# Kernel optimization log

Measured on AMD Instinct MI355X. Metric: run time of the kernel, lower is better.

Reference implementation:

```python
import jax, jax.numpy as jnp
import numpy as np

B, S, D, H = 8, 1024, 768, 12
DH = D // H
EPS = 1e-5


def setup_inputs() -> dict:
    key = jax.random.key(0)
    ks = jax.random.split(key, 12)
    sc_h = 1.0 / np.sqrt(DH)
    sc_d = 1.0 / np.sqrt(D)
    return {
        "x": jax.random.normal(ks[0], (B, S, D), jnp.float32),
        "ln1_g": jnp.ones((D,), jnp.float32),
        "ln1_b": jnp.zeros((D,), jnp.float32),
        "Wq": jax.random.normal(ks[1], (H, DH, DH), jnp.float32) * sc_h,
        "bq": jax.random.normal(ks[2], (H, DH), jnp.float32) * 0.01,
        "Wk": jax.random.normal(ks[3], (H, DH, DH), jnp.float32) * sc_h,
        "bk": jax.random.normal(ks[4], (H, DH), jnp.float32) * 0.01,
        "Wv": jax.random.normal(ks[5], (H, DH, DH), jnp.float32) * sc_h,
        "bv": jax.random.normal(ks[6], (H, DH), jnp.float32) * 0.01,
        "ln2_g": jnp.ones((D,), jnp.float32),
        "ln2_b": jnp.zeros((D,), jnp.float32),
        "W1": jax.random.normal(ks[7], (D, 4 * D), jnp.float32) * sc_d,  # c_fc (bias=False)
        "W2": jax.random.normal(ks[8], (4 * D, D), jnp.float32) * (1.0 / np.sqrt(4 * D)),  # c_proj (bias=False)
    }


def _layernorm(x, g, b):
    m = jnp.mean(x, axis=-1, keepdims=True)
    v = jnp.mean(jnp.square(x - m), axis=-1, keepdims=True)
    return (x - m) * jax.lax.rsqrt(v + EPS) * g + b


def _msa(x, Wq, bq, Wk, bk, Wv, bv):
    b, s, d = x.shape
    h = x.reshape(b, s, H, DH)  # per-head slices of the embedding
    q = jnp.einsum('bshd,hde->bhse', h, Wq) + bq[None, :, None, :]
    k = jnp.einsum('bshd,hde->bhse', h, Wk) + bk[None, :, None, :]
    v = jnp.einsum('bshd,hde->bhse', h, Wv) + bv[None, :, None, :]
    scores = jnp.einsum('bhse,bhte->bhst', q, k) / np.sqrt(DH).astype(np.float32)
    attn = jax.nn.softmax(scores, axis=-1)
    o = jnp.einsum('bhst,bhte->bhse', attn, v)
    return o.transpose(0, 2, 1, 3).reshape(b, s, d)  # concat heads


def reference(x, ln1_g, ln1_b, Wq, bq, Wk, bk, Wv, bv, ln2_g, ln2_b, W1, W2):
    out = x + _msa(_layernorm(x, ln1_g, ln1_b), Wq, bq, Wk, bk, Wv, bv)
    h = _layernorm(out, ln2_g, ln2_b)
    ffn = jnp.dot(jax.nn.gelu(jnp.dot(h, W1), approximate=False), W2)
    return out + ffn
```

## Files before the change

kernel.cpp:

```cpp
#include <hip/hip_runtime.h>
#include <hip/hip_bf16.h>
#include <math.h>

#define B_ 8
#define S_ 1024
#define D_ 768
#define H_ 12
#define QSCALE 0.18033688011112042f

typedef __attribute__((ext_vector_type(8))) short short8;
typedef __attribute__((ext_vector_type(4))) float floatx4;
typedef unsigned short ushort_t;

__device__ __forceinline__ ushort_t f2bf(float f) {
  unsigned int u = __builtin_bit_cast(unsigned int, f);
  u += 0x7fffu + ((u >> 16) & 1u);
  return (ushort_t)(u >> 16);
}

__device__ __forceinline__ unsigned int pkbf(float a, float b) {
  __hip_bfloat162 h = __float22bfloat162_rn(make_float2(a, b));
  unsigned int r;
  __builtin_memcpy(&r, &h, sizeof(r));
  return r;
}

__global__ __launch_bounds__(256) void ln_bf16(
    const float* __restrict__ in, const float* __restrict__ g,
    const float* __restrict__ bias, ushort_t* __restrict__ out) {
  const int row = blockIdx.x * 4 + (threadIdx.x >> 6);
  const int lane = threadIdx.x & 63;
  const float* p = in + (size_t)row * D_;
  float4 v[3];
#pragma unroll
  for (int j = 0; j < 3; ++j) v[j] = *(const float4*)(p + j * 256 + lane * 4);
  float s = 0.f;
#pragma unroll
  for (int j = 0; j < 3; ++j) s += (v[j].x + v[j].y) + (v[j].z + v[j].w);
#pragma unroll
  for (int m = 1; m < 64; m <<= 1) s += __shfl_xor(s, m);
  const float mean = s * (1.0f / D_);
  float q = 0.f;
#pragma unroll
  for (int j = 0; j < 3; ++j) {
    const float a = v[j].x - mean, b = v[j].y - mean;
    const float c = v[j].z - mean, d = v[j].w - mean;
    q += (a * a + b * b) + (c * c + d * d);
  }
#pragma unroll
  for (int m = 1; m < 64; m <<= 1) q += __shfl_xor(q, m);
  const float rstd = rsqrtf(q * (1.0f / D_) + 1e-5f);
  ushort_t* o = out + (size_t)row * D_;
#pragma unroll
  for (int j = 0; j < 3; ++j) {
    const float4 gv = *(const float4*)(g + j * 256 + lane * 4);
    const float4 bv = *(const float4*)(bias + j * 256 + lane * 4);
    const unsigned int p01 = pkbf((v[j].x - mean) * rstd * gv.x + bv.x,
                                  (v[j].y - mean) * rstd * gv.y + bv.y);
    const unsigned int p23 = pkbf((v[j].z - mean) * rstd * gv.z + bv.z,
                                  (v[j].w - mean) * rstd * gv.w + bv.w);
    *(uint2*)(o + j * 256 + lane * 4) = make_uint2(p01, p23);
  }
}

__global__ __launch_bounds__(256) void transpose_cast(
    const float* __restrict__ W, ushort_t* __restrict__ Wt, int Kdim, int Ndim) {
  __shared__ float tile[32][33];
  const int n0 = blockIdx.x * 32, k0 = blockIdx.y * 32;
  const int tx = threadIdx.x & 31, ty = threadIdx.x >> 5;
#pragma unroll
  for (int i = 0; i < 32; i += 8)
    tile[ty + i][tx] = W[(size_t)(k0 + ty + i) * Ndim + n0 + tx];
  __syncthreads();
#pragma unroll
  for (int i = 0; i < 32; i += 8)
    Wt[(size_t)(n0 + ty + i) * Kdim + k0 + tx] = f2bf(tile[tx][ty + i]);
}

__global__ __launch_bounds__(256) void trans_w64(
    const float* __restrict__ Wq, const float* __restrict__ Wk,
    const float* __restrict__ Wv, ushort_t* __restrict__ Wqt,
    ushort_t* __restrict__ Wkt, ushort_t* __restrict__ Wvt) {
  const int h = blockIdx.x;
  const float* W = blockIdx.y == 0 ? Wq : blockIdx.y == 1 ? Wk : Wv;
  ushort_t* O = blockIdx.y == 0 ? Wqt : blockIdx.y == 1 ? Wkt : Wvt;
  __shared__ float t[64][65];
  const int tid = threadIdx.x;
#pragma unroll
  for (int i = 0; i < 16; ++i) {
    const int idx = tid + i * 256;
    t[idx >> 6][idx & 63] = W[h * 4096 + idx];
  }
  __syncthreads();
#pragma unroll
  for (int i = 0; i < 16; ++i) {
    const int idx = tid + i * 256;
    O[h * 4096 + idx] = f2bf(t[idx & 63][idx >> 6]);
  }
}

__global__ __launch_bounds__(256) void qkv_mfma(
    const ushort_t* __restrict__ xbf,
    const ushort_t* __restrict__ Wqt, const ushort_t* __restrict__ Wkt,
    const ushort_t* __restrict__ Wvt,
    const float* __restrict__ bq, const float* __restrict__ bk,
    const float* __restrict__ bv,
    ushort_t* __restrict__ qo, ushort_t* __restrict__ ko,
    ushort_t* __restrict__ vt) {
  const int h = blockIdx.y;
  const int mb = blockIdx.x * 128;
  const int tid = threadIdx.x;
  const int wave = tid >> 6, lane = tid & 63;
  const int lc = lane & 15, kq = lane >> 4;
  const int wm = wave * 32;

  short8 af[2][2];
#pragma unroll
  for (int mi = 0; mi < 2; ++mi)
#pragma unroll
    for (int kc = 0; kc < 2; ++kc)
      af[mi][kc] = *(const short8*)(xbf + (size_t)(mb + wm + mi * 16 + lc) * D_ +
                                    h * 64 + kc * 32 + kq * 8);

  const ushort_t* Wp[3] = {Wqt + h * 4096, Wkt + h * 4096, Wvt + h * 4096};
  floatx4 acc[3][2][4] = {};
#pragma unroll
  for (int w3 = 0; w3 < 3; ++w3)
#pragma unroll
    for (int n = 0; n < 4; ++n)
#pragma unroll
      for (int kc = 0; kc < 2; ++kc) {
        const short8 bfv =
            *(const short8*)(Wp[w3] + (n * 16 + lc) * 64 + kc * 32 + kq * 8);
#pragma unroll
        for (int mi = 0; mi < 2; ++mi)
          acc[w3][mi][n] = __builtin_amdgcn_mfma_f32_16x16x32_bf16(
              af[mi][kc], bfv, acc[w3][mi][n], 0, 0, 0);
      }

  const int b = mb >> 10;
  const size_t obase = (size_t)(b * H_ + h) * (S_ * 64);
#pragma unroll
  for (int w3 = 0; w3 < 2; ++w3) {
    const float* bias = (w3 == 0 ? bq : bk) + h * 64;
    ushort_t* outp = w3 == 0 ? qo : ko;
#pragma unroll
    for (int n = 0; n < 4; ++n) {
      const int e = n * 16 + lc;
      const float bvv = bias[e];
#pragma unroll
      for (int mi = 0; mi < 2; ++mi)
#pragma unroll
        for (int r = 0; r < 4; ++r) {
          const int sl = (mb & 1023) + wm + mi * 16 + kq * 4 + r;
          float v = acc[w3][mi][n][r] + bvv;
          if (w3 == 0) v *= QSCALE;
          outp[obase + (size_t)sl * 64 + e] = f2bf(v);
        }
    }
  }
#pragma unroll
  for (int n = 0; n < 4; ++n) {
    const int e = n * 16 + lc;
    const float bvv = bv[h * 64 + e];
#pragma unroll
    for (int mi = 0; mi < 2; ++mi) {
      const int sl0 = (mb & 1023) + wm + mi * 16 + kq * 4;
      const unsigned int p01 =
          pkbf(acc[2][mi][n][0] + bvv, acc[2][mi][n][1] + bvv);
      const unsigned int p23 =
          pkbf(acc[2][mi][n][2] + bvv, acc[2][mi][n][3] + bvv);
      *(uint2*)(vt + obase + (size_t)e * S_ + sl0) = make_uint2(p01, p23);
    }
  }
}

__global__ __launch_bounds__(256) void attn_mfma(
    const ushort_t* __restrict__ qb, const ushort_t* __restrict__ kb,
    const ushort_t* __restrict__ vt, const float* __restrict__ x,
    float* __restrict__ out1) {
  const int bh = blockIdx.x;
  const int tid = threadIdx.x;
  const int wave = tid >> 6, lane = tid & 63;
  const int lc = lane & 15, kq = lane >> 4;
  const int q0 = blockIdx.y * 128 + wave * 32;

  __shared__ __align__(16) ushort_t Ks[64 * 64];
  __shared__ __align__(16) ushort_t Vs[64 * 64];
  __shared__ __align__(16) ushort_t Pw[4][2][16 * 72];

  const ushort_t* qp = qb + (size_t)bh * (S_ * 64);
  const ushort_t* kp = kb + (size_t)bh * (S_ * 64);
  const ushort_t* vp = vt + (size_t)bh * (S_ * 64);

  short8 qf[2][2];
#pragma unroll
  for (int qi = 0; qi < 2; ++qi)
#pragma unroll
    for (int kc = 0; kc < 2; ++kc)
      qf[qi][kc] = *(const short8*)(qp + (size_t)(q0 + qi * 16 + lc) * 64 +
                                    kc * 32 + kq * 8);

  const int srow = tid >> 3;
  const int sgc = ((tid & 7) ^ (srow & 7)) * 8;
  const int slds = srow * 64 + (tid & 7) * 8;
  const int swz = lc & 7;

  float l_r[2] = {0.0f, 0.0f};
  floatx4 oacc[2][4] = {};

  for (int kt = 0; kt < 16; ++kt) {
#pragma unroll
    for (int half = 0; half < 2; ++half) {
      const int r = half * 32 + srow;
      __builtin_amdgcn_global_load_lds(
          (const __attribute__((address_space(1))) unsigned int*)
              (kp + (size_t)(kt * 64 + r) * 64 + sgc),
          (__attribute__((address_space(3))) unsigned int*)
              (Ks + half * 2048 + slds), 16, 0, 0);
      __builtin_amdgcn_global_load_lds(
          (const __attribute__((address_space(1))) unsigned int*)
              (vp + (size_t)r * S_ + kt * 64 + sgc),
          (__attribute__((address_space(3))) unsigned int*)
              (Vs + half * 2048 + slds), 16, 0, 0);
    }
    __syncthreads();

    floatx4 sacc[2][4] = {};
#pragma unroll
    for (int mi = 0; mi < 4; ++mi) {
      const int row = (mi * 16 + lc) * 64;
#pragma unroll
      for (int kc = 0; kc < 2; ++kc) {
        const short8 kf =
            *(const short8*)(Ks + row + ((kc * 4 + kq) ^ swz) * 8);
        sacc[0][mi] = __builtin_amdgcn_mfma_f32_16x16x32_bf16(
            kf, qf[0][kc], sacc[0][mi], 0, 0, 0);
        sacc[1][mi] = __builtin_amdgcn_mfma_f32_16x16x32_bf16(
            kf, qf[1][kc], sacc[1][mi], 0, 0, 0);
      }
    }

#pragma unroll
    for (int qi = 0; qi < 2; ++qi) {
      float pr[4][4];
      float sm = 0.f;
#pragma unroll
      for (int mi = 0; mi < 4; ++mi)
#pragma unroll
        for (int r = 0; r < 4; ++r) {
          pr[mi][r] = exp2f(sacc[qi][mi][r]);
          sm += pr[mi][r];
        }
      l_r[qi] += sm;
#pragma unroll
      for (int mi = 0; mi < 4; ++mi) {
        const unsigned int p01 = pkbf(pr[mi][0], pr[mi][1]);
        const unsigned int p23 = pkbf(pr[mi][2], pr[mi][3]);
        *(uint2*)(&Pw[wave][qi][lc * 72 + mi * 16 + kq * 4]) =
            make_uint2(p01, p23);
      }
    }
    asm volatile("s_waitcnt lgkmcnt(0)" ::: "memory");

    short8 pf[2][2];
#pragma unroll
    for (int qi = 0; qi < 2; ++qi)
#pragma unroll
      for (int kc = 0; kc < 2; ++kc)
        pf[qi][kc] =
            *(const short8*)(&Pw[wave][qi][lc * 72 + kc * 32 + kq * 8]);
#pragma unroll
    for (int mi = 0; mi < 4; ++mi) {
      const int row = (mi * 16 + lc) * 64;
#pragma unroll
      for (int kc = 0; kc < 2; ++kc) {
        const short8 vf =
            *(const short8*)(Vs + row + ((kc * 4 + kq) ^ swz) * 8);
        oacc[0][mi] = __builtin_amdgcn_mfma_f32_16x16x32_bf16(
            vf, pf[0][kc], oacc[0][mi], 0, 0, 0);
        oacc[1][mi] = __builtin_amdgcn_mfma_f32_16x16x32_bf16(
            vf, pf[1][kc], oacc[1][mi], 0, 0, 0);
      }
    }
    __syncthreads();
  }

  const int b = bh / H_, h = bh % H_;
  float* Ow = (float*)&Pw[wave][0][0];
#pragma unroll
  for (int qi = 0; qi < 2; ++qi) {
    float lt = l_r[qi];
    lt += __shfl_xor(lt, 16);
    lt += __shfl_xor(lt, 32);
    const float inv = 1.0f / lt;
#pragma unroll
    for (int mi = 0; mi < 4; ++mi) {
      floatx4 ov = oacc[qi][mi];
      ov[0] *= inv; ov[1] *= inv; ov[2] *= inv; ov[3] *= inv;
      *(floatx4*)(&Ow[lc * 68 + mi * 16 + kq * 4]) = ov;
    }
    asm volatile("s_waitcnt lgkmcnt(0)" ::: "memory");
    const int row = (lane >> 3) & 7, c8 = (lane & 7) * 4;
#pragma unroll
    for (int rg = 0; rg < 2; ++rg) {
      const int qq = rg * 8 + row;
      const size_t gbase =
          ((size_t)(b * S_) + q0 + qi * 16 + qq) * D_ + h * 64 + c8;
#pragma unroll
      for (int j = 0; j < 2; ++j) {
        const float4 ov = *(const float4*)(&Ow[qq * 68 + j * 32 + c8]);
        const float4 xv = *(const float4*)(x + gbase + j * 32);
        *(float4*)(out1 + gbase + j * 32) =
            make_float4(ov.x + xv.x, ov.y + xv.y, ov.z + xv.z, ov.w + xv.w);
      }
    }
    asm volatile("s_waitcnt lgkmcnt(0)" ::: "memory");
  }
}

template <int N, int K, bool GELU, bool RESID, bool OUT_BF16>
__global__ __launch_bounds__(256) void mfma_gemm(
    const ushort_t* __restrict__ A, const ushort_t* __restrict__ Bt,
    const float* __restrict__ resid, void* __restrict__ Cout) {
  const int mb = blockIdx.y * 128;
  const int nb = blockIdx.x * 128;
  const int tid = threadIdx.x;
  const int wave = tid >> 6, lane = tid & 63;
  const int wm = (wave >> 1) * 64, wn = (wave & 1) * 64;

  __shared__ ushort_t Asp[128 * 32];
  __shared__ ushort_t Bsp[128 * 32];

  const int srow = wave * 16 + (lane >> 2);
  const int skoff = (lane & 3) * 8;

  floatx4 acc[4][4] = {};

  for (int kb = 0; kb < K; kb += 32) {
#pragma unroll
    for (int j = 0; j < 2; ++j) {
      const int row = j * 64 + srow;
      __builtin_amdgcn_global_load_lds(
          (const __attribute__((address_space(1))) unsigned int*)
              (A + (size_t)(mb + row) * K + kb + skoff),
          (__attribute__((address_space(3))) unsigned int*)
              (Asp + (size_t)row * 32 + skoff),
          16, 0, 0);
      __builtin_amdgcn_global_load_lds(
          (const __attribute__((address_space(1))) unsigned int*)
              (Bt + (size_t)(nb + row) * K + kb + skoff),
          (__attribute__((address_space(3))) unsigned int*)
              (Bsp + (size_t)row * 32 + skoff),
          16, 0, 0);
    }
    __syncthreads();

    const short8* As8 = (const short8*)Asp;
    const short8* Bs8 = (const short8*)Bsp;
    const int lrow = lane & 15, lkq = lane >> 4;
    short8 af[4], bfr[4];
#pragma unroll
    for (int i = 0; i < 4; ++i) {
      af[i]  = As8[(wm + i * 16 + lrow) * 4 + lkq];
      bfr[i] = Bs8[(wn + i * 16 + lrow) * 4 + lkq];
    }
#pragma unroll
    for (int i = 0; i < 4; ++i)
#pragma unroll
      for (int j = 0; j < 4; ++j)
        acc[i][j] = __builtin_amdgcn_mfma_f32_16x16x32_bf16(
            af[i], bfr[j], acc[i][j], 0, 0, 0);
    __syncthreads();
  }

  const int lcol = lane & 15, lr4 = (lane >> 4) * 4;
#pragma unroll
  for (int i = 0; i < 4; ++i)
#pragma unroll
    for (int r = 0; r < 4; ++r) {
      const int m = mb + wm + i * 16 + lr4 + r;
#pragma unroll
      for (int j = 0; j < 4; ++j) {
        const int col = nb + wn + j * 16 + lcol;
        float vv = acc[i][j][r];
        if (GELU) vv = 0.5f * vv * (1.0f + erff(vv * 0.70710678f));
        if (RESID) vv += resid[(size_t)m * N + col];
        if (OUT_BF16)
          ((ushort_t*)Cout)[(size_t)m * N + col] = f2bf(vv);
        else
          ((float*)Cout)[(size_t)m * N + col] = vv;
      }
    }
}

template <int N, int K>
__global__ __launch_bounds__(256) void mfma_gemm2(
    const ushort_t* __restrict__ A, const ushort_t* __restrict__ Bt,
    const float* __restrict__ resid, float* __restrict__ C) {
  const int mb = blockIdx.y * 64;
  const int nb = blockIdx.x * 128;
  const int tid = threadIdx.x;
  const int wave = tid >> 6, lane = tid & 63;
  const int wm = (wave >> 1) * 32, wn = (wave & 1) * 64;

  __shared__ ushort_t Asp[64 * 32];
  __shared__ ushort_t Bsp[128 * 32];

  const int srow = wave * 16 + (lane >> 2);
  const int skoff = (lane & 3) * 8;

  floatx4 acc[2][4] = {};

  for (int kb = 0; kb < K; kb += 32) {
    __builtin_amdgcn_global_load_lds(
        (const __attribute__((address_space(1))) unsigned int*)
            (A + (size_t)(mb + srow) * K + kb + skoff),
        (__attribute__((address_space(3))) unsigned int*)
            (Asp + (size_t)srow * 32 + skoff),
        16, 0, 0);
#pragma unroll
    for (int j = 0; j < 2; ++j) {
      const int row = j * 64 + srow;
      __builtin_amdgcn_global_load_lds(
          (const __attribute__((address_space(1))) unsigned int*)
              (Bt + (size_t)(nb + row) * K + kb + skoff),
          (__attribute__((address_space(3))) unsigned int*)
              (Bsp + (size_t)row * 32 + skoff),
          16, 0, 0);
    }
    __syncthreads();

    const short8* As8 = (const short8*)Asp;
    const short8* Bs8 = (const short8*)Bsp;
    const int lrow = lane & 15, lkq = lane >> 4;
    short8 af[2], bfr[4];
#pragma unroll
    for (int i = 0; i < 2; ++i) af[i] = As8[(wm + i * 16 + lrow) * 4 + lkq];
#pragma unroll
    for (int j = 0; j < 4; ++j) bfr[j] = Bs8[(wn + j * 16 + lrow) * 4 + lkq];
#pragma unroll
    for (int i = 0; i < 2; ++i)
#pragma unroll
      for (int j = 0; j < 4; ++j)
        acc[i][j] = __builtin_amdgcn_mfma_f32_16x16x32_bf16(
            af[i], bfr[j], acc[i][j], 0, 0, 0);
    __syncthreads();
  }

  const int lcol = lane & 15, lr4 = (lane >> 4) * 4;
#pragma unroll
  for (int i = 0; i < 2; ++i)
#pragma unroll
    for (int r = 0; r < 4; ++r) {
      const int m = mb + wm + i * 16 + lr4 + r;
#pragma unroll
      for (int j = 0; j < 4; ++j) {
        const int col = nb + wn + j * 16 + lcol;
        C[(size_t)m * N + col] =
            acc[i][j][r] + resid[(size_t)m * N + col];
      }
    }
}

extern "C" void kernel_launch(void* const* d_in, const int* in_sizes, int n_in,
                              void* d_out, int out_size, void* d_ws, size_t ws_size,
                              hipStream_t stream) {
  (void)in_sizes; (void)n_in; (void)out_size; (void)ws_size;
  const float* x     = (const float*)d_in[0];
  const float* ln1_g = (const float*)d_in[1];
  const float* ln1_b = (const float*)d_in[2];
  const float* Wq    = (const float*)d_in[3];
  const float* bq    = (const float*)d_in[4];
  const float* Wk    = (const float*)d_in[5];
  const float* bk    = (const float*)d_in[6];
  const float* Wv    = (const float*)d_in[7];
  const float* bv    = (const float*)d_in[8];
  const float* ln2_g = (const float*)d_in[9];
  const float* ln2_b = (const float*)d_in[10];
  const float* W1    = (const float*)d_in[11];
  const float* W2    = (const float*)d_in[12];
  float* out = (float*)d_out;

  const size_t n = (size_t)B_ * S_ * D_;
  ushort_t* u = (ushort_t*)d_ws;
  ushort_t* xbf  = u;
  ushort_t* qb   = xbf + n;
  ushort_t* kb   = qb + n;
  ushort_t* vt   = kb + n;
  ushort_t* xbf2 = vt + n;
  ushort_t* act  = xbf2 + n;
  ushort_t* Wt1  = act + (size_t)8192 * 3072;
  ushort_t* Wt2  = Wt1 + (size_t)3072 * 768;
  ushort_t* Wqt  = Wt2 + (size_t)768 * 3072;
  ushort_t* Wkt  = Wqt + H_ * 4096;
  ushort_t* Wvt  = Wkt + H_ * 4096;
  float* out1 = (float*)(Wvt + H_ * 4096);

  trans_w64<<<dim3(12, 3), dim3(256), 0, stream>>>(Wq, Wk, Wv, Wqt, Wkt, Wvt);
  transpose_cast<<<dim3(96, 24), dim3(256), 0, stream>>>(W1, Wt1, 768, 3072);
  transpose_cast<<<dim3(24, 96), dim3(256), 0, stream>>>(W2, Wt2, 3072, 768);
  ln_bf16<<<dim3(2048), dim3(256), 0, stream>>>(x, ln1_g, ln1_b, xbf);
  qkv_mfma<<<dim3(64, 12), dim3(256), 0, stream>>>(xbf, Wqt, Wkt, Wvt,
                                                   bq, bk, bv, qb, kb, vt);
  attn_mfma<<<dim3(96, 8), dim3(256), 0, stream>>>(qb, kb, vt, x, out1);
  ln_bf16<<<dim3(2048), dim3(256), 0, stream>>>(out1, ln2_g, ln2_b, xbf2);
  mfma_gemm<3072, 768, true, false, true>
      <<<dim3(24, 64), dim3(256), 0, stream>>>(xbf2, Wt1, nullptr, act);
  mfma_gemm2<768, 3072>
      <<<dim3(6, 128), dim3(256), 0, stream>>>(act, Wt2, out1, out);
}
```

Before: 342.9 us.

## Deepen K tile, swizzle LDS, and remap blocks per XCD in second FFN GEMM

The down-projection GEMM now stages a 64-wide K slice per iteration instead of 32. This halves the number of barrier pairs and issues two MFMA k-steps per sync. LDS rows are XOR-swizzled on the global-to-LDS load side and read back with the matching swizzle to avoid bank conflicts on the 128-byte row stride. The grid is flattened to 1D and remapped so that each XCD handles a contiguous band of 16 M-blocks across all 6 N-blocks, which improves L2 reuse of A rows. LDS use doubles, which may reduce occupancy slightly.

```diff
diff --git a/kernel.cpp b/kernel.cpp
--- a/kernel.cpp
+++ b/kernel.cpp
@@ -398,53 +398,67 @@
 __global__ __launch_bounds__(256) void mfma_gemm2(
     const ushort_t* __restrict__ A, const ushort_t* __restrict__ Bt,
     const float* __restrict__ resid, float* __restrict__ C) {
-  const int mb = blockIdx.y * 64;
-  const int nb = blockIdx.x * 128;
+  const int lin = blockIdx.x;
+  const int xcd = lin & 7, slot = lin >> 3;
+  const int mbg = slot / 6, nbi = slot - mbg * 6;
+  const int mb = (xcd * 16 + mbg) * 64;
+  const int nb = nbi * 128;
   const int tid = threadIdx.x;
   const int wave = tid >> 6, lane = tid & 63;
   const int wm = (wave >> 1) * 32, wn = (wave & 1) * 64;
 
-  __shared__ ushort_t Asp[64 * 32];
-  __shared__ ushort_t Bsp[128 * 32];
-
-  const int srow = wave * 16 + (lane >> 2);
-  const int skoff = (lane & 3) * 8;
+  __shared__ __align__(16) ushort_t Asp[64 * 64];
+  __shared__ __align__(16) ushort_t Bsp[128 * 64];
+
+  const int sr = tid >> 3;
+  const int sc8 = (tid & 7) * 8;
+  const int sgx = ((tid & 7) ^ (sr & 7)) * 8;
 
   floatx4 acc[2][4] = {};
 
-  for (int kb = 0; kb < K; kb += 32) {
-    __builtin_amdgcn_global_load_lds(
-        (const __attribute__((address_space(1))) unsigned int*)
-            (A + (size_t)(mb + srow) * K + kb + skoff),
-        (__attribute__((address_space(3))) unsigned int*)
-            (Asp + (size_t)srow * 32 + skoff),
-        16, 0, 0);
+  for (int kb = 0; kb < K; kb += 64) {
 #pragma unroll
     for (int j = 0; j < 2; ++j) {
-      const int row = j * 64 + srow;
+      const int row = j * 32 + sr;
       __builtin_amdgcn_global_load_lds(
           (const __attribute__((address_space(1))) unsigned int*)
-              (Bt + (size_t)(nb + row) * K + kb + skoff),
+              (A + (size_t)(mb + row) * K + kb + sgx),
           (__attribute__((address_space(3))) unsigned int*)
-              (Bsp + (size_t)row * 32 + skoff),
-          16, 0, 0);
+              (Asp + row * 64 + sc8), 16, 0, 0);
+    }
+#pragma unroll
+    for (int j = 0; j < 4; ++j) {
+      const int row = j * 32 + sr;
+      __builtin_amdgcn_global_load_lds(
+          (const __attribute__((address_space(1))) unsigned int*)
+              (Bt + (size_t)(nb + row) * K + kb + sgx),
+          (__attribute__((address_space(3))) unsigned int*)
+              (Bsp + row * 64 + sc8), 16, 0, 0);
     }
     __syncthreads();
 
-    const short8* As8 = (const short8*)Asp;
-    const short8* Bs8 = (const short8*)Bsp;
-    const int lrow = lane & 15, lkq = lane >> 4;
-    short8 af[2], bfr[4];
-#pragma unroll
-    for (int i = 0; i < 2; ++i) af[i] = As8[(wm + i * 16 + lrow) * 4 + lkq];
-#pragma unroll
-    for (int j = 0; j < 4; ++j) bfr[j] = Bs8[(wn + j * 16 + lrow) * 4 + lkq];
+    const int lc = lane & 15, kq = lane >> 4, swz = lc & 7;
+    short8 af[2][2], bfr[4][2];
 #pragma unroll
     for (int i = 0; i < 2; ++i)
 #pragma unroll
-      for (int j = 0; j < 4; ++j)
-        acc[i][j] = __builtin_amdgcn_mfma_f32_16x16x32_bf16(
-            af[i], bfr[j], acc[i][j], 0, 0, 0);
+      for (int ks = 0; ks < 2; ++ks)
+        af[i][ks] = *(const short8*)(Asp + (wm + i * 16 + lc) * 64 +
+                                     ((ks * 4 + kq) ^ swz) * 8);
+#pragma unroll
+    for (int j = 0; j < 4; ++j)
+#pragma unroll
+      for (int ks = 0; ks < 2; ++ks)
+        bfr[j][ks] = *(const short8*)(Bsp + (wn + j * 16 + lc) * 64 +
+                                      ((ks * 4 + kq) ^ swz) * 8);
+#pragma unroll
+    for (int ks = 0; ks < 2; ++ks)
+#pragma unroll
+      for (int i = 0; i < 2; ++i)
+#pragma unroll
+        for (int j = 0; j < 4; ++j)
+          acc[i][j] = __builtin_amdgcn_mfma_f32_16x16x32_bf16(
+              af[i][ks], bfr[j][ks], acc[i][j], 0, 0, 0);
     __syncthreads();
   }
 
@@ -508,5 +522,5 @@
   mfma_gemm<3072, 768, true, false, true>
       <<<dim3(24, 64), dim3(256), 0, stream>>>(xbf2, Wt1, nullptr, act);
   mfma_gemm2<768, 3072>
-      <<<dim3(6, 128), dim3(256), 0, stream>>>(act, Wt2, out1, out);
-}
+      <<<dim3(768), dim3(256), 0, stream>>>(act, Wt2, out1, out);
+}
```

New measurement: 309.0 us. 1.11x faster.
